# Kernel tuning notes

Measured on AMD Instinct MI355X. Metric: run time of the kernel, lower is better.

Reference implementation:

```python
import jax, jax.numpy as jnp
import numpy as np

N_NODES = 100000


def _gcn_conv(x, W, b, src, dst, deg_inv_sqrt):
    # linear transform first (PyG GCNConv order): [N, F] @ [F, H]
    h = x @ W
    # symmetric normalization per edge: deg^-1/2[src] * deg^-1/2[dst]
    norm = deg_inv_sqrt[src] * deg_inv_sqrt[dst]
    msg = h[src] * norm[:, None]  # [E, H]
    out = jax.ops.segment_sum(msg, dst, num_segments=N_NODES)
    return out + b


def setup_inputs() -> dict:
    key = jax.random.key(0)
    k1, k2, k3, k4 = jax.random.split(key, 4)
    F_IN, H = 512, 512
    E = 800000
    x = jax.random.normal(k1, (N_NODES, F_IN), dtype=jnp.float32)
    edge_index = jax.random.randint(k2, (2, E), 0, N_NODES, dtype=jnp.int64)
    W1 = jax.random.normal(k3, (F_IN, H), dtype=jnp.float32) * (1.0 / np.sqrt(F_IN))
    b1 = jnp.zeros((H,), dtype=jnp.float32)
    W2 = jax.random.normal(k4, (H, H), dtype=jnp.float32) * (1.0 / np.sqrt(H))
    b2 = jnp.zeros((H,), dtype=jnp.float32)
    return {"x": x, "edge_index": edge_index, "W1": W1, "b1": b1, "W2": W2, "b2": b2}


def reference(x, edge_index, W1, b1, W2, b2):
    # add self loops (PyG GCNConv default add_self_loops=True)
    loop = jnp.arange(N_NODES, dtype=edge_index.dtype)
    src = jnp.concatenate([edge_index[0], loop])
    dst = jnp.concatenate([edge_index[1], loop])
    # degree of destination nodes (including self loops)
    deg = jax.ops.segment_sum(jnp.ones_like(dst, dtype=x.dtype), dst, num_segments=N_NODES)
    deg_inv_sqrt = jnp.where(deg > 0, jax.lax.rsqrt(jnp.maximum(deg, 1.0)), 0.0)
    h = jax.nn.relu(_gcn_conv(x, W1, b1, src, dst, deg_inv_sqrt))
    # dropout is identity at inference (training=False)
    out = _gcn_conv(h, W2, b2, src, dst, deg_inv_sqrt)
    return out
```

## Files before the change

### kernel.cpp

```cpp
#include <hip/hip_runtime.h>

#define N_NODES 100000
#define E_EDGES 800000
#define E_TOT   900000
#define F 512

typedef __attribute__((ext_vector_type(8))) short short8;
typedef __attribute__((ext_vector_type(4))) float f32x4;
typedef unsigned int u32;

__device__ __forceinline__ float bfu(unsigned int u) {
    union { unsigned int i; float f; } c; c.i = u << 16; return c.f;
}
__device__ __forceinline__ unsigned short f2b(float f) {
    union { float f; unsigned int u; } c; c.f = f;
    return (unsigned short)((c.u + 0x7fffu + ((c.u >> 16) & 1u)) >> 16);
}
__device__ __forceinline__ void gload_lds16(const void* g, void* l) {
    __builtin_amdgcn_global_load_lds(
        (const __attribute__((address_space(1))) u32*)g,
        (__attribute__((address_space(3))) u32*)l, 16, 0, 0);
}

__global__ void k_init(unsigned int* deg, unsigned int* counter) {
    int i = blockIdx.x * 256 + threadIdx.x;
    if (i < N_NODES) deg[i] = 1u;
    if (i == 0) *counter = 0u;
}

__global__ void k_hist(const int* __restrict__ ei, unsigned int* deg) {
    int e = blockIdx.x * 256 + threadIdx.x;
    if (e < E_EDGES) atomicAdd(&deg[ei[E_EDGES + e]], 1u);
}

__global__ void k_dis(const unsigned int* __restrict__ deg, float* __restrict__ dis) {
    int i = blockIdx.x * 256 + threadIdx.x;
    if (i < N_NODES) dis[i] = rsqrtf((float)deg[i]);
}

__global__ void k_alloc(const unsigned int* __restrict__ deg, unsigned int* counter,
                        int* __restrict__ rs, unsigned int* __restrict__ cursor) {
    int i = blockIdx.x * 256 + threadIdx.x;
    if (i < N_NODES) {
        unsigned int p = atomicAdd(counter, deg[i]);
        rs[i] = (int)p;
        cursor[i] = p;
    }
}

__global__ void k_scatter(const int* __restrict__ ei, const float* __restrict__ dis,
                          unsigned int* __restrict__ cursor,
                          int* __restrict__ col, float* __restrict__ val) {
    int e = blockIdx.x * 256 + threadIdx.x;
    if (e < E_TOT) {
        int s, d;
        if (e < E_EDGES) { s = ei[e]; d = ei[E_EDGES + e]; }
        else             { s = e - E_EDGES; d = s; }
        unsigned int p = atomicAdd(&cursor[d], 1u);
        col[p] = s;
        val[p] = dis[s] * dis[d];
    }
}

__global__ void k_cvtX(const float* __restrict__ xin, unsigned short* __restrict__ xb) {
    int i = blockIdx.x * 256 + threadIdx.x;
    const float4* p = (const float4*)xin + (size_t)i * 2;
    float4 a = p[0], b = p[1];
    uint4 o;
    o.x = (unsigned)f2b(a.x) | ((unsigned)f2b(a.y) << 16);
    o.y = (unsigned)f2b(a.z) | ((unsigned)f2b(a.w) << 16);
    o.z = (unsigned)f2b(b.x) | ((unsigned)f2b(b.y) << 16);
    o.w = (unsigned)f2b(b.z) | ((unsigned)f2b(b.w) << 16);
    *(uint4*)(xb + (size_t)i * 8) = o;
}

__global__ void k_cvtW(const float* __restrict__ W, unsigned short* __restrict__ Wt) {
    int t = blockIdx.x * 256 + threadIdx.x;
    if (t < F * F) {
        int n = t >> 9, k = t & 511;
        Wt[t] = f2b(W[k * F + n]);
    }
}

__global__ __launch_bounds__(256)
void gemm_bt(const unsigned short* __restrict__ A, const unsigned short* __restrict__ Bt,
             unsigned short* __restrict__ C, int M) {
    __shared__ unsigned short lsa[128 * 64];
    __shared__ unsigned short lsb[128 * 64];
    int bx = blockIdx.x;
    int by = blockIdx.y;
    int t  = threadIdx.x;
    int lane = t & 63, w = t >> 6;
    int wr = w >> 1, wc = w & 1;

    f32x4 acc[4][4];
    #pragma unroll
    for (int m = 0; m < 4; ++m)
        #pragma unroll
        for (int n = 0; n < 4; ++n)
            acc[m][n] = (f32x4){0.f, 0.f, 0.f, 0.f};

    int rowBase = bx * 128;

    int ar[4], akc[4], br[4];
    #pragma unroll
    for (int i = 0; i < 4; ++i) {
        int idx = i * 256 + t;
        int r = idx >> 3;
        akc[i] = (idx & 7) * 8;
        int ga = rowBase + r; if (ga >= M) ga = M - 1;
        ar[i] = ga;
        br[i] = by * 128 + r;
    }

    for (int k0 = 0; k0 < F; k0 += 64) {
        #pragma unroll
        for (int i = 0; i < 4; ++i) {
            int idx = i * 256 + t;
            gload_lds16(A + (size_t)ar[i] * F + k0 + akc[i], lsa + idx * 8);
            gload_lds16(Bt + (size_t)br[i] * F + k0 + akc[i], lsb + idx * 8);
        }
        __syncthreads();
        #pragma unroll
        for (int ks = 0; ks < 2; ++ks) {
            int koff = ks * 32 + (lane >> 4) * 8;
            short8 af[4], bfr[4];
            #pragma unroll
            for (int m = 0; m < 4; ++m)
                af[m] = *(short8*)&lsa[(wr * 64 + m * 16 + (lane & 15)) * 64 + koff];
            #pragma unroll
            for (int n = 0; n < 4; ++n)
                bfr[n] = *(short8*)&lsb[(wc * 64 + n * 16 + (lane & 15)) * 64 + koff];
            #pragma unroll
            for (int m = 0; m < 4; ++m)
                #pragma unroll
                for (int n = 0; n < 4; ++n)
                    acc[m][n] = __builtin_amdgcn_mfma_f32_16x16x32_bf16(af[m], bfr[n], acc[m][n], 0, 0, 0);
        }
        __syncthreads();
    }

    int rq = (lane >> 4) * 4, cq = lane & 15;
    #pragma unroll
    for (int m = 0; m < 4; ++m)
        #pragma unroll
        for (int n = 0; n < 4; ++n)
            #pragma unroll
            for (int j = 0; j < 4; ++j) {
                int row = rowBase + wr * 64 + m * 16 + rq + j;
                if (row < M) {
                    int colv = by * 128 + wc * 64 + n * 16 + cq;
                    C[(size_t)row * F + colv] = f2b(acc[m][n][j]);
                }
            }
}

__global__ __launch_bounds__(256)
void k_agg(const unsigned short* __restrict__ hin, const int* __restrict__ rs,
           const unsigned int* __restrict__ deg,
           const int* __restrict__ col, const float* __restrict__ val,
           const float* __restrict__ bias,
           unsigned short* __restrict__ outb, float* __restrict__ outf, int relu) {
    int node = blockIdx.x * 4 + (threadIdx.x >> 6);
    int lane = threadIdx.x & 63;
    if (node >= N_NODES) return;
    int e0 = rs[node], e1 = e0 + (int)deg[node];
    float acc[8] = {0, 0, 0, 0, 0, 0, 0, 0};
    for (int e = e0; e < e1; ++e) {
        int s = col[e];
        float wv = val[e];
        uint4 v = *(const uint4*)(hin + (size_t)s * F + lane * 8);
        acc[0] += wv * bfu(v.x & 0xffffu);
        acc[1] += wv * bfu(v.x >> 16);
        acc[2] += wv * bfu(v.y & 0xffffu);
        acc[3] += wv * bfu(v.y >> 16);
        acc[4] += wv * bfu(v.z & 0xffffu);
        acc[5] += wv * bfu(v.z >> 16);
        acc[6] += wv * bfu(v.w & 0xffffu);
        acc[7] += wv * bfu(v.w >> 16);
    }
    #pragma unroll
    for (int j = 0; j < 8; ++j) {
        acc[j] += bias[lane * 8 + j];
        if (relu) acc[j] = fmaxf(acc[j], 0.f);
    }
    if (outb) {
        uint4 o;
        o.x = (unsigned)f2b(acc[0]) | ((unsigned)f2b(acc[1]) << 16);
        o.y = (unsigned)f2b(acc[2]) | ((unsigned)f2b(acc[3]) << 16);
        o.z = (unsigned)f2b(acc[4]) | ((unsigned)f2b(acc[5]) << 16);
        o.w = (unsigned)f2b(acc[6]) | ((unsigned)f2b(acc[7]) << 16);
        *(uint4*)(outb + (size_t)node * F + lane * 8) = o;
    } else {
        f32x4 o1 = {acc[0], acc[1], acc[2], acc[3]};
        f32x4 o2 = {acc[4], acc[5], acc[6], acc[7]};
        f32x4* p = (f32x4*)(outf + (size_t)node * F + lane * 8);
        __builtin_nontemporal_store(o1, p);
        __builtin_nontemporal_store(o2, p + 1);
    }
}

extern "C" void kernel_launch(void* const* d_in, const int* in_sizes, int n_in,
                              void* d_out, int out_size, void* d_ws, size_t ws_size,
                              hipStream_t stream) {
    const float* x  = (const float*)d_in[0];
    const int*   ei = (const int*)d_in[1];
    const float* W1 = (const float*)d_in[2];
    const float* b1 = (const float*)d_in[3];
    const float* W2 = (const float*)d_in[4];
    const float* b2 = (const float*)d_in[5];
    float* out = (float*)d_out;

    char* ws = (char*)d_ws;
    size_t off = 0;
    auto alloc = [&](size_t bytes) -> void* {
        off = (off + 255) & ~(size_t)255;
        void* p = ws + off;
        off += bytes;
        return p;
    };

    unsigned short* tb  = (unsigned short*)alloc((size_t)N_NODES * F * 2);
    unsigned short* W1t = (unsigned short*)alloc((size_t)F * F * 2);
    unsigned short* W2t = (unsigned short*)alloc((size_t)F * F * 2);
    unsigned int*   deg = (unsigned int*)alloc((size_t)N_NODES * 4);
    float*          dis = (float*)alloc((size_t)N_NODES * 4);
    int*            rs  = (int*)alloc((size_t)N_NODES * 4);
    unsigned int*   cur = (unsigned int*)alloc((size_t)N_NODES * 4);
    unsigned int*   cnt = (unsigned int*)alloc(256);
    int*            col = (int*)alloc((size_t)E_TOT * 4);
    float*          val = (float*)alloc((size_t)E_TOT * 4);

    unsigned short* h1b = (unsigned short*)d_out;
    unsigned short* xb  = (unsigned short*)((char*)d_out + (size_t)N_NODES * F * 2);

    int nb = (N_NODES + 255) / 256;

    k_init<<<nb, 256, 0, stream>>>(deg, cnt);
    k_hist<<<(E_EDGES + 255) / 256, 256, 0, stream>>>(ei, deg);
    k_dis<<<nb, 256, 0, stream>>>(deg, dis);
    k_alloc<<<nb, 256, 0, stream>>>(deg, cnt, rs, cur);
    k_scatter<<<(E_TOT + 255) / 256, 256, 0, stream>>>(ei, dis, cur, col, val);

    k_cvtW<<<(F * F + 255) / 256, 256, 0, stream>>>(W1, W1t);
    k_cvtW<<<(F * F + 255) / 256, 256, 0, stream>>>(W2, W2t);
    k_cvtX<<<(N_NODES * F / 8) / 256, 256, 0, stream>>>(x, xb);

    dim3 ggrid((N_NODES + 127) / 128, F / 128);

    gemm_bt<<<ggrid, 256, 0, stream>>>(xb, W1t, tb, N_NODES);
    k_agg<<<(N_NODES + 3) / 4, 256, 0, stream>>>(tb, rs, deg, col, val, b1, h1b, nullptr, 1);

    gemm_bt<<<ggrid, 256, 0, stream>>>(h1b, W2t, tb, N_NODES);
    k_agg<<<(N_NODES + 3) / 4, 256, 0, stream>>>(tb, rs, deg, col, val, b2, nullptr, out, 0);
}
```

Baseline: 673.4 us.

## Aggregate before GEMM, fuse bias/ReLU into GEMM epilogue, double-buffer LDS

Reorders each GCN layer to aggregate the features first (A·X) and then apply the weight matrix, using associativity. Bias and ReLU move into the GEMM epilogue, which now writes either bf16 or fp32 output directly. The GEMM K-loop gains double-buffered LDS staging so global loads can overlap the MFMA work. The aggregation kernel splits the feature dimension across two grid columns with 4-wide loads, which adds an extra rounding of the aggregated features to bf16 before the GEMM. The fp32 output is now written with scalar strided nontemporal stores instead of vectorized ones.

```diff
diff --git a/kernel.cpp b/kernel.cpp
--- a/kernel.cpp
+++ b/kernel.cpp
@@ -84,9 +84,11 @@
 
 __global__ __launch_bounds__(256)
 void gemm_bt(const unsigned short* __restrict__ A, const unsigned short* __restrict__ Bt,
-             unsigned short* __restrict__ C, int M) {
-    __shared__ unsigned short lsa[128 * 64];
-    __shared__ unsigned short lsb[128 * 64];
+             const float* __restrict__ bias,
+             unsigned short* __restrict__ outb, float* __restrict__ outf,
+             int relu, int M) {
+    __shared__ unsigned short lsa[2][128 * 64];
+    __shared__ unsigned short lsb[2][128 * 64];
     int bx = blockIdx.x;
     int by = blockIdx.y;
     int t  = threadIdx.x;
@@ -113,24 +115,31 @@
         br[i] = by * 128 + r;
     }
 
-    for (int k0 = 0; k0 < F; k0 += 64) {
+    auto STAGE = [&](int buf, int k0) {
         #pragma unroll
         for (int i = 0; i < 4; ++i) {
             int idx = i * 256 + t;
-            gload_lds16(A + (size_t)ar[i] * F + k0 + akc[i], lsa + idx * 8);
-            gload_lds16(Bt + (size_t)br[i] * F + k0 + akc[i], lsb + idx * 8);
+            gload_lds16(A + (size_t)ar[i] * F + k0 + akc[i], &lsa[buf][idx * 8]);
+            gload_lds16(Bt + (size_t)br[i] * F + k0 + akc[i], &lsb[buf][idx * 8]);
         }
-        __syncthreads();
+    };
+
+    STAGE(0, 0);
+    __syncthreads();
+    #pragma unroll 2
+    for (int kt = 0; kt < 8; ++kt) {
+        int cur = kt & 1;
+        if (kt < 7) STAGE(cur ^ 1, (kt + 1) * 64);
         #pragma unroll
         for (int ks = 0; ks < 2; ++ks) {
             int koff = ks * 32 + (lane >> 4) * 8;
             short8 af[4], bfr[4];
             #pragma unroll
             for (int m = 0; m < 4; ++m)
-                af[m] = *(short8*)&lsa[(wr * 64 + m * 16 + (lane & 15)) * 64 + koff];
+                af[m] = *(short8*)&lsa[cur][(wr * 64 + m * 16 + (lane & 15)) * 64 + koff];
             #pragma unroll
             for (int n = 0; n < 4; ++n)
-                bfr[n] = *(short8*)&lsb[(wc * 64 + n * 16 + (lane & 15)) * 64 + koff];
+                bfr[n] = *(short8*)&lsb[cur][(wc * 64 + n * 16 + (lane & 15)) * 64 + koff];
             #pragma unroll
             for (int m = 0; m < 4; ++m)
                 #pragma unroll
@@ -144,60 +153,47 @@
     #pragma unroll
     for (int m = 0; m < 4; ++m)
         #pragma unroll
-        for (int n = 0; n < 4; ++n)
+        for (int n = 0; n < 4; ++n) {
+            int colv = by * 128 + wc * 64 + n * 16 + cq;
+            float bv = bias[colv];
             #pragma unroll
             for (int j = 0; j < 4; ++j) {
                 int row = rowBase + wr * 64 + m * 16 + rq + j;
                 if (row < M) {
-                    int colv = by * 128 + wc * 64 + n * 16 + cq;
-                    C[(size_t)row * F + colv] = f2b(acc[m][n][j]);
+                    float v = acc[m][n][j] + bv;
+                    if (relu) v = fmaxf(v, 0.f);
+                    if (outb) outb[(size_t)row * F + colv] = f2b(v);
+                    else __builtin_nontemporal_store(v, outf + (size_t)row * F + colv);
                 }
             }
+        }
 }
 
 __global__ __launch_bounds__(256)
-void k_agg(const unsigned short* __restrict__ hin, const int* __restrict__ rs,
-           const unsigned int* __restrict__ deg,
-           const int* __restrict__ col, const float* __restrict__ val,
-           const float* __restrict__ bias,
-           unsigned short* __restrict__ outb, float* __restrict__ outf, int relu) {
+void k_agg2(const unsigned short* __restrict__ hin, const int* __restrict__ rs,
+            const unsigned int* __restrict__ deg,
+            const int* __restrict__ col, const float* __restrict__ val,
+            unsigned short* __restrict__ outb) {
     int node = blockIdx.x * 4 + (threadIdx.x >> 6);
     int lane = threadIdx.x & 63;
+    int coff = blockIdx.y * 256 + lane * 4;
     if (node >= N_NODES) return;
     int e0 = rs[node], e1 = e0 + (int)deg[node];
-    float acc[8] = {0, 0, 0, 0, 0, 0, 0, 0};
+    float a0 = 0.f, a1 = 0.f, a2 = 0.f, a3 = 0.f;
+    const unsigned short* base = hin + coff;
     for (int e = e0; e < e1; ++e) {
         int s = col[e];
         float wv = val[e];
-        uint4 v = *(const uint4*)(hin + (size_t)s * F + lane * 8);
-        acc[0] += wv * bfu(v.x & 0xffffu);
-        acc[1] += wv * bfu(v.x >> 16);
-        acc[2] += wv * bfu(v.y & 0xffffu);
-        acc[3] += wv * bfu(v.y >> 16);
-        acc[4] += wv * bfu(v.z & 0xffffu);
-        acc[5] += wv * bfu(v.z >> 16);
-        acc[6] += wv * bfu(v.w & 0xffffu);
-        acc[7] += wv * bfu(v.w >> 16);
-    }
-    #pragma unroll
-    for (int j = 0; j < 8; ++j) {
-        acc[j] += bias[lane * 8 + j];
-        if (relu) acc[j] = fmaxf(acc[j], 0.f);
-    }
-    if (outb) {
-        uint4 o;
-        o.x = (unsigned)f2b(acc[0]) | ((unsigned)f2b(acc[1]) << 16);
-        o.y = (unsigned)f2b(acc[2]) | ((unsigned)f2b(acc[3]) << 16);
-        o.z = (unsigned)f2b(acc[4]) | ((unsigned)f2b(acc[5]) << 16);
-        o.w = (unsigned)f2b(acc[6]) | ((unsigned)f2b(acc[7]) << 16);
-        *(uint4*)(outb + (size_t)node * F + lane * 8) = o;
-    } else {
-        f32x4 o1 = {acc[0], acc[1], acc[2], acc[3]};
-        f32x4 o2 = {acc[4], acc[5], acc[6], acc[7]};
-        f32x4* p = (f32x4*)(outf + (size_t)node * F + lane * 8);
-        __builtin_nontemporal_store(o1, p);
-        __builtin_nontemporal_store(o2, p + 1);
-    }
+        uint2 v = *(const uint2*)(base + (size_t)s * F);
+        a0 += wv * bfu(v.x & 0xffffu);
+        a1 += wv * bfu(v.x >> 16);
+        a2 += wv * bfu(v.y & 0xffffu);
+        a3 += wv * bfu(v.y >> 16);
+    }
+    uint2 o;
+    o.x = (unsigned)f2b(a0) | ((unsigned)f2b(a1) << 16);
+    o.y = (unsigned)f2b(a2) | ((unsigned)f2b(a3) << 16);
+    *(uint2*)(outb + (size_t)node * F + coff) = o;
 }
 
 extern "C" void kernel_launch(void* const* d_in, const int* in_sizes, int n_in,
@@ -247,10 +243,11 @@
     k_cvtX<<<(N_NODES * F / 8) / 256, 256, 0, stream>>>(x, xb);
 
     dim3 ggrid((N_NODES + 127) / 128, F / 128);
-
-    gemm_bt<<<ggrid, 256, 0, stream>>>(xb, W1t, tb, N_NODES);
-    k_agg<<<(N_NODES + 3) / 4, 256, 0, stream>>>(tb, rs, deg, col, val, b1, h1b, nullptr, 1);
-
-    gemm_bt<<<ggrid, 256, 0, stream>>>(h1b, W2t, tb, N_NODES);
-    k_agg<<<(N_NODES + 3) / 4, 256, 0, stream>>>(tb, rs, deg, col, val, b2, nullptr, out, 0);
-}
+    dim3 agrid((N_NODES + 3) / 4, 2);
+
+    k_agg2<<<agrid, 256, 0, stream>>>(xb, rs, deg, col, val, tb);
+    gemm_bt<<<ggrid, 256, 0, stream>>>(tb, W1t, b1, h1b, nullptr, 1, N_NODES);
+
+    k_agg2<<<agrid, 256, 0, stream>>>(h1b, rs, deg, col, val, tb);
+    gemm_bt<<<ggrid, 256, 0, stream>>>(tb, W2t, b2, nullptr, out, 0, N_NODES);
+}
```

Measured after the change: 892.4 us. 1.33x slower.

## Aggregate before GEMM and fuse bias/ReLU into GEMM epilogue; pack edge arrays

Applied to the files above, without the earlier changes.

Reorders each GCN layer to aggregate neighbour features first and then apply the linear transform, using linearity (A·X·W = (A·X)·W). The bias, ReLU and final fp32 output move into the GEMM epilogue. Column index and weight are packed into one uint2 per edge, segment bounds into int2, and the gather loop is unrolled by four for more loads in flight. The cost is an extra bf16 rounding of the aggregated input before the GEMM, which changes numerics slightly. The GEMM epilogue now writes fp32 output with scalar strided stores instead of vectorised ones.

```diff
diff --git a/kernel.cpp b/kernel.cpp
--- a/kernel.cpp
+++ b/kernel.cpp
@@ -16,6 +16,12 @@
     union { float f; unsigned int u; } c; c.f = f;
     return (unsigned short)((c.u + 0x7fffu + ((c.u >> 16) & 1u)) >> 16);
 }
+__device__ __forceinline__ float fbits(unsigned int u) {
+    union { unsigned int i; float f; } c; c.i = u; return c.f;
+}
+__device__ __forceinline__ unsigned int bits(float f) {
+    union { float f; unsigned int i; } c; c.f = f; return c.i;
+}
 __device__ __forceinline__ void gload_lds16(const void* g, void* l) {
     __builtin_amdgcn_global_load_lds(
         (const __attribute__((address_space(1))) u32*)g,
@@ -39,26 +45,26 @@
 }
 
 __global__ void k_alloc(const unsigned int* __restrict__ deg, unsigned int* counter,
-                        int* __restrict__ rs, unsigned int* __restrict__ cursor) {
+                        int2* __restrict__ seg, unsigned int* __restrict__ cursor) {
     int i = blockIdx.x * 256 + threadIdx.x;
     if (i < N_NODES) {
-        unsigned int p = atomicAdd(counter, deg[i]);
-        rs[i] = (int)p;
+        unsigned int d = deg[i];
+        unsigned int p = atomicAdd(counter, d);
+        seg[i] = make_int2((int)p, (int)(p + d));
         cursor[i] = p;
     }
 }
 
 __global__ void k_scatter(const int* __restrict__ ei, const float* __restrict__ dis,
                           unsigned int* __restrict__ cursor,
-                          int* __restrict__ col, float* __restrict__ val) {
+                          uint2* __restrict__ ev) {
     int e = blockIdx.x * 256 + threadIdx.x;
     if (e < E_TOT) {
         int s, d;
         if (e < E_EDGES) { s = ei[e]; d = ei[E_EDGES + e]; }
         else             { s = e - E_EDGES; d = s; }
         unsigned int p = atomicAdd(&cursor[d], 1u);
-        col[p] = s;
-        val[p] = dis[s] * dis[d];
+        ev[p] = make_uint2((unsigned)s, bits(dis[s] * dis[d]));
     }
 }
 
@@ -84,7 +90,9 @@
 
 __global__ __launch_bounds__(256)
 void gemm_bt(const unsigned short* __restrict__ A, const unsigned short* __restrict__ Bt,
-             unsigned short* __restrict__ C, int M) {
+             const float* __restrict__ bias,
+             unsigned short* __restrict__ outb, float* __restrict__ outf,
+             int relu, int M) {
     __shared__ unsigned short lsa[128 * 64];
     __shared__ unsigned short lsb[128 * 64];
     int bx = blockIdx.x;
@@ -144,60 +152,75 @@
     #pragma unroll
     for (int m = 0; m < 4; ++m)
         #pragma unroll
-        for (int n = 0; n < 4; ++n)
+        for (int n = 0; n < 4; ++n) {
+            int colv = by * 128 + wc * 64 + n * 16 + cq;
+            float bv = bias[colv];
             #pragma unroll
             for (int j = 0; j < 4; ++j) {
                 int row = rowBase + wr * 64 + m * 16 + rq + j;
                 if (row < M) {
-                    int colv = by * 128 + wc * 64 + n * 16 + cq;
-                    C[(size_t)row * F + colv] = f2b(acc[m][n][j]);
+                    float v = acc[m][n][j] + bv;
+                    if (relu) v = fmaxf(v, 0.f);
+                    if (outb) outb[(size_t)row * F + colv] = f2b(v);
+                    else __builtin_nontemporal_store(v, outf + (size_t)row * F + colv);
                 }
             }
+        }
 }
 
 __global__ __launch_bounds__(256)
-void k_agg(const unsigned short* __restrict__ hin, const int* __restrict__ rs,
-           const unsigned int* __restrict__ deg,
-           const int* __restrict__ col, const float* __restrict__ val,
-           const float* __restrict__ bias,
-           unsigned short* __restrict__ outb, float* __restrict__ outf, int relu) {
+void k_agg(const unsigned short* __restrict__ hin, const int2* __restrict__ seg,
+           const uint2* __restrict__ ev,
+           unsigned short* __restrict__ outb) {
     int node = blockIdx.x * 4 + (threadIdx.x >> 6);
     int lane = threadIdx.x & 63;
     if (node >= N_NODES) return;
-    int e0 = rs[node], e1 = e0 + (int)deg[node];
+    int2 se = seg[node];
+    int e0 = se.x, e1 = se.y;
     float acc[8] = {0, 0, 0, 0, 0, 0, 0, 0};
-    for (int e = e0; e < e1; ++e) {
-        int s = col[e];
-        float wv = val[e];
-        uint4 v = *(const uint4*)(hin + (size_t)s * F + lane * 8);
-        acc[0] += wv * bfu(v.x & 0xffffu);
-        acc[1] += wv * bfu(v.x >> 16);
-        acc[2] += wv * bfu(v.y & 0xffffu);
-        acc[3] += wv * bfu(v.y >> 16);
-        acc[4] += wv * bfu(v.z & 0xffffu);
-        acc[5] += wv * bfu(v.z >> 16);
-        acc[6] += wv * bfu(v.w & 0xffffu);
-        acc[7] += wv * bfu(v.w >> 16);
-    }
-    #pragma unroll
-    for (int j = 0; j < 8; ++j) {
-        acc[j] += bias[lane * 8 + j];
-        if (relu) acc[j] = fmaxf(acc[j], 0.f);
-    }
-    if (outb) {
-        uint4 o;
-        o.x = (unsigned)f2b(acc[0]) | ((unsigned)f2b(acc[1]) << 16);
-        o.y = (unsigned)f2b(acc[2]) | ((unsigned)f2b(acc[3]) << 16);
-        o.z = (unsigned)f2b(acc[4]) | ((unsigned)f2b(acc[5]) << 16);
-        o.w = (unsigned)f2b(acc[6]) | ((unsigned)f2b(acc[7]) << 16);
-        *(uint4*)(outb + (size_t)node * F + lane * 8) = o;
-    } else {
-        f32x4 o1 = {acc[0], acc[1], acc[2], acc[3]};
-        f32x4 o2 = {acc[4], acc[5], acc[6], acc[7]};
-        f32x4* p = (f32x4*)(outf + (size_t)node * F + lane * 8);
-        __builtin_nontemporal_store(o1, p);
-        __builtin_nontemporal_store(o2, p + 1);
-    }
+    const unsigned short* base = hin + lane * 8;
+
+    int e = e0;
+    for (; e + 3 < e1; e += 4) {
+        uint2 p0 = ev[e], p1 = ev[e + 1], p2 = ev[e + 2], p3 = ev[e + 3];
+        uint4 v0 = *(const uint4*)(base + ((size_t)p0.x << 9));
+        uint4 v1 = *(const uint4*)(base + ((size_t)p1.x << 9));
+        uint4 v2 = *(const uint4*)(base + ((size_t)p2.x << 9));
+        uint4 v3 = *(const uint4*)(base + ((size_t)p3.x << 9));
+        float w0 = fbits(p0.y), w1 = fbits(p1.y), w2 = fbits(p2.y), w3 = fbits(p3.y);
+        acc[0] += w0 * bfu(v0.x & 0xffffu); acc[1] += w0 * bfu(v0.x >> 16);
+        acc[2] += w0 * bfu(v0.y & 0xffffu); acc[3] += w0 * bfu(v0.y >> 16);
+        acc[4] += w0 * bfu(v0.z & 0xffffu); acc[5] += w0 * bfu(v0.z >> 16);
+        acc[6] += w0 * bfu(v0.w & 0xffffu); acc[7] += w0 * bfu(v0.w >> 16);
+        acc[0] += w1 * bfu(v1.x & 0xffffu); acc[1] += w1 * bfu(v1.x >> 16);
+        acc[2] += w1 * bfu(v1.y & 0xffffu); acc[3] += w1 * bfu(v1.y >> 16);
+        acc[4] += w1 * bfu(v1.z & 0xffffu); acc[5] += w1 * bfu(v1.z >> 16);
+        acc[6] += w1 * bfu(v1.w & 0xffffu); acc[7] += w1 * bfu(v1.w >> 16);
+        acc[0] += w2 * bfu(v2.x & 0xffffu); acc[1] += w2 * bfu(v2.x >> 16);
+        acc[2] += w2 * bfu(v2.y & 0xffffu); acc[3] += w2 * bfu(v2.y >> 16);
+        acc[4] += w2 * bfu(v2.z & 0xffffu); acc[5] += w2 * bfu(v2.z >> 16);
+        acc[6] += w2 * bfu(v2.w & 0xffffu); acc[7] += w2 * bfu(v2.w >> 16);
+        acc[0] += w3 * bfu(v3.x & 0xffffu); acc[1] += w3 * bfu(v3.x >> 16);
+        acc[2] += w3 * bfu(v3.y & 0xffffu); acc[3] += w3 * bfu(v3.y >> 16);
+        acc[4] += w3 * bfu(v3.z & 0xffffu); acc[5] += w3 * bfu(v3.z >> 16);
+        acc[6] += w3 * bfu(v3.w & 0xffffu); acc[7] += w3 * bfu(v3.w >> 16);
+    }
+    for (; e < e1; ++e) {
+        uint2 p = ev[e];
+        uint4 v = *(const uint4*)(base + ((size_t)p.x << 9));
+        float wv = fbits(p.y);
+        acc[0] += wv * bfu(v.x & 0xffffu); acc[1] += wv * bfu(v.x >> 16);
+        acc[2] += wv * bfu(v.y & 0xffffu); acc[3] += wv * bfu(v.y >> 16);
+        acc[4] += wv * bfu(v.z & 0xffffu); acc[5] += wv * bfu(v.z >> 16);
+        acc[6] += wv * bfu(v.w & 0xffffu); acc[7] += wv * bfu(v.w >> 16);
+    }
+
+    uint4 o;
+    o.x = (unsigned)f2b(acc[0]) | ((unsigned)f2b(acc[1]) << 16);
+    o.y = (unsigned)f2b(acc[2]) | ((unsigned)f2b(acc[3]) << 16);
+    o.z = (unsigned)f2b(acc[4]) | ((unsigned)f2b(acc[5]) << 16);
+    o.w = (unsigned)f2b(acc[6]) | ((unsigned)f2b(acc[7]) << 16);
+    *(uint4*)(outb + (size_t)node * F + lane * 8) = o;
 }
 
 extern "C" void kernel_launch(void* const* d_in, const int* in_sizes, int n_in,
@@ -225,11 +248,10 @@
     unsigned short* W2t = (unsigned short*)alloc((size_t)F * F * 2);
     unsigned int*   deg = (unsigned int*)alloc((size_t)N_NODES * 4);
     float*          dis = (float*)alloc((size_t)N_NODES * 4);
-    int*            rs  = (int*)alloc((size_t)N_NODES * 4);
+    int2*           seg = (int2*)alloc((size_t)N_NODES * 8);
     unsigned int*   cur = (unsigned int*)alloc((size_t)N_NODES * 4);
     unsigned int*   cnt = (unsigned int*)alloc(256);
-    int*            col = (int*)alloc((size_t)E_TOT * 4);
-    float*          val = (float*)alloc((size_t)E_TOT * 4);
+    uint2*          ev  = (uint2*)alloc((size_t)E_TOT * 8);
 
     unsigned short* h1b = (unsigned short*)d_out;
     unsigned short* xb  = (unsigned short*)((char*)d_out + (size_t)N_NODES * F * 2);
@@ -239,8 +261,8 @@
     k_init<<<nb, 256, 0, stream>>>(deg, cnt);
     k_hist<<<(E_EDGES + 255) / 256, 256, 0, stream>>>(ei, deg);
     k_dis<<<nb, 256, 0, stream>>>(deg, dis);
-    k_alloc<<<nb, 256, 0, stream>>>(deg, cnt, rs, cur);
-    k_scatter<<<(E_TOT + 255) / 256, 256, 0, stream>>>(ei, dis, cur, col, val);
+    k_alloc<<<nb, 256, 0, stream>>>(deg, cnt, seg, cur);
+    k_scatter<<<(E_TOT + 255) / 256, 256, 0, stream>>>(ei, dis, cur, ev);
 
     k_cvtW<<<(F * F + 255) / 256, 256, 0, stream>>>(W1, W1t);
     k_cvtW<<<(F * F + 255) / 256, 256, 0, stream>>>(W2, W2t);
@@ -248,9 +270,9 @@
 
     dim3 ggrid((N_NODES + 127) / 128, F / 128);
 
-    gemm_bt<<<ggrid, 256, 0, stream>>>(xb, W1t, tb, N_NODES);
-    k_agg<<<(N_NODES + 3) / 4, 256, 0, stream>>>(tb, rs, deg, col, val, b1, h1b, nullptr, 1);
-
-    gemm_bt<<<ggrid, 256, 0, stream>>>(h1b, W2t, tb, N_NODES);
-    k_agg<<<(N_NODES + 3) / 4, 256, 0, stream>>>(tb, rs, deg, col, val, b2, nullptr, out, 0);
-}
+    k_agg<<<(N_NODES + 3) / 4, 256, 0, stream>>>(xb, seg, ev, tb);
+    gemm_bt<<<ggrid, 256, 0, stream>>>(tb, W1t, b1, h1b, nullptr, 1, N_NODES);
+
+    k_agg<<<(N_NODES + 3) / 4, 256, 0, stream>>>(h1b, seg, ev, tb);
+    gemm_bt<<<ggrid, 256, 0, stream>>>(tb, W2t, b2, nullptr, out, 0, N_NODES);
+}
```

New measurement: 723.9 us. 7.5% more time.
